# Kernel tuning notes

Measured on AMD Instinct MI355X. Metric: run time of the kernel, lower is better.

## Reference

```python
import jax, jax.numpy as jnp
import numpy as np

NSAMPLE = 16
LEAKY_RATE = 0.1


def _knn(xyz, k):
    # xyz: [B,N,3] -> idx of k nearest neighbors (incl. self): [B,N,k]
    sq = jnp.sum(xyz * xyz, axis=-1)  # [B,N]
    dist = sq[:, :, None] + sq[:, None, :] - 2.0 * jnp.einsum('bnd,bmd->bnm', xyz, xyz)
    _, idx = jax.lax.top_k(-dist, k)
    return idx


def _gather(feat, idx):
    # feat [B,N,C], idx [B,N,K] -> [B,N,K,C]
    return jax.vmap(lambda f, i: f[i])(feat, idx)


def setup_inputs() -> dict:
    key = jax.random.key(0)
    ks = jax.random.split(key, 10)
    B, N, D = 8, 4096, 61
    in_ch, out_ch, wnet = 64, 64, 16
    inp = {
        'xyz': jax.random.normal(ks[0], (B, 3, N), dtype=jnp.float32),
        'points': jax.random.normal(ks[1], (B, D, N), dtype=jnp.float32),
        # WeightNet: 1x1 convs 3->8->8->16 (hidden_unit=[8,8]), no BN
        'w0': jax.random.normal(ks[2], (8, 3), dtype=jnp.float32) * 0.3,
        'b0': jnp.zeros((8,), dtype=jnp.float32),
        'w1': jax.random.normal(ks[3], (8, 8), dtype=jnp.float32) * 0.3,
        'b1': jnp.zeros((8,), dtype=jnp.float32),
        'w2': jax.random.normal(ks[4], (wnet, 8), dtype=jnp.float32) * 0.3,
        'b2': jnp.zeros((wnet,), dtype=jnp.float32),
        # final Linear: weightnet*in_channel -> out_channel (torch [out,in] layout)
        'lin_w': jax.random.normal(ks[5], (out_ch, wnet * in_ch), dtype=jnp.float32) * 0.03,
        'lin_b': jnp.zeros((out_ch,), dtype=jnp.float32),
    }
    return inp


def reference(xyz, points, w0, b0, w1, b1, w2, b2, lin_w, lin_b):
    B, _, N = xyz.shape
    xyz_t = jnp.transpose(xyz, (0, 2, 1))     # [B,N,3]
    pts_t = jnp.transpose(points, (0, 2, 1))  # [B,N,D]
    idx = _knn(xyz_t, NSAMPLE)                # [B,N,K]
    g_xyz = _gather(xyz_t, idx) - xyz_t[:, :, None, :]   # [B,N,K,3] relative coords
    g_pts = _gather(pts_t, idx)                           # [B,N,K,D]
    new_points = jnp.concatenate([g_xyz, g_pts], axis=-1)  # [B,N,K,C], C=D+3
    # WeightNet: per-neighbor 1x1-conv MLP with ReLU on relative coords
    h = jax.nn.relu(jnp.einsum('bnkc,oc->bnko', g_xyz, w0) + b0)
    h = jax.nn.relu(jnp.einsum('bnkc,oc->bnko', h, w1) + b1)
    w = jax.nn.relu(jnp.einsum('bnkc,oc->bnko', h, w2) + b2)  # [B,N,K,W]
    # aggregate: [B,N,C,K] @ [B,N,K,W] -> [B,N,C,W] -> flatten C*W (W fastest)
    agg = jnp.einsum('bnkc,bnkw->bncw', new_points, w).reshape(B, N, -1)
    out = agg @ lin_w.T + lin_b          # [B,N,out_ch]
    out = jnp.transpose(out, (0, 2, 1))  # [B,out_ch,N]
    return jnp.where(out > 0, out, LEAKY_RATE * out)  # LeakyReLU(0.1)
```

## Files before the change

### kernel.cpp

```cpp
#include <hip/hip_runtime.h>
#include <hip/hip_bf16.h>

#define NBATCH 8
#define NP     4096
#define ND     61
#define NK     16
#define BN     (NBATCH*NP)

#define OFF_XYZT  0
#define OFF_IDX   (OFF_XYZT + BN*16)
#define OFF_PTST  (OFF_IDX + BN*64)
#define OFF_BFRAG (OFF_PTST + BN*256)

typedef __attribute__((ext_vector_type(8))) short bf16x8;
typedef __attribute__((ext_vector_type(4))) float f32x4;

static __device__ __forceinline__ unsigned short f2bf(float x) {
    unsigned int u = __float_as_uint(x);
    return (unsigned short)((u + 0x7fffu + ((u >> 16) & 1u)) >> 16);
}

__global__ __launch_bounds__(256) void k_prep_xyz(const float* __restrict__ xyz,
                                                  float4* __restrict__ xyzt) {
#pragma clang fp contract(off)
    int t = blockIdx.x * 256 + threadIdx.x;
    int b = t >> 12, n = t & (NP - 1);
    const float* base = xyz + (size_t)b * 3 * NP + n;
    float x = base[0], y = base[NP], z = base[2 * NP];
    float sq = ((x * x) + (y * y)) + (z * z);
    xyzt[t] = make_float4(x, y, z, sq);
}

__global__ __launch_bounds__(256) void k_prep_ptst(const float* __restrict__ pts,
                                                   float* __restrict__ ptst) {
    __shared__ float tile[64][65];
    int blk = blockIdx.x;
    int b = blk >> 6; int n0 = (blk & 63) << 6;
    int tid = threadIdx.x; int rg = tid >> 6; int cl = tid & 63;
#pragma unroll
    for (int d0 = 0; d0 < 64; d0 += 4) {
        int d = d0 + rg;
        if (d < ND) tile[d][cl] = pts[((size_t)b * ND + d) * NP + n0 + cl];
    }
    __syncthreads();
#pragma unroll
    for (int r = 0; r < 16; ++r) {
        int n1 = r * 4 + rg;
        float v = (cl < ND) ? tile[cl][n1] : 0.0f;
        ptst[((size_t)b * NP + n0 + n1) * 64 + cl] = v;
    }
}

__global__ __launch_bounds__(256) void k_prep_bfrag(const float* __restrict__ lw,
                                                    uint4* __restrict__ bfrag) {
    int e = blockIdx.x * 256 + threadIdx.x;
    int lane = e & 63, nt = (e >> 6) & 3, ks = e >> 8;
    int k0 = ks * 32 + (lane >> 4) * 8;
    int n = nt * 16 + (lane & 15);
    const float* src = lw + (size_t)n * 1024 + k0;
    unsigned int pk[4];
#pragma unroll
    for (int i = 0; i < 4; ++i)
        pk[i] = ((unsigned int)f2bf(src[2 * i + 1]) << 16) | f2bf(src[2 * i]);
    bfrag[e] = make_uint4(pk[0], pk[1], pk[2], pk[3]);
}

#define INSERT16(dv, jv)                                            \
    do {                                                            \
        bd[15] = (dv); bi[15] = (jv);                               \
        _Pragma("unroll")                                           \
        for (int s_ = 15; s_ > 0; --s_) {                           \
            bool sw_ = bd[s_] < bd[s_ - 1];                         \
            float td_ = bd[s_]; int ti_ = bi[s_];                   \
            bd[s_]     = sw_ ? bd[s_ - 1] : td_;                    \
            bi[s_]     = sw_ ? bi[s_ - 1] : ti_;                    \
            bd[s_ - 1] = sw_ ? td_ : bd[s_ - 1];                    \
            bi[s_ - 1] = sw_ ? ti_ : bi[s_ - 1];                    \
        }                                                           \
    } while (0)

#define DRAIN16(basev)                                                        \
    do {                                                                      \
        for (int r_ = 0; r_ < 16; ++r_) {                                     \
            if (!__any(r_ < cnt)) break;                                      \
            if (r_ < cnt) {                                                   \
                int loc_ = ring[r_ * 64 + lane];                              \
                float4 cd_ = tile[loc_];                                      \
                float dot_ = __fadd_rn(__fadd_rn(__fmul_rn(cd_.x, me.x),      \
                                                 __fmul_rn(cd_.y, me.y)),     \
                                       __fmul_rn(cd_.z, me.z));               \
                float dist_ = __fsub_rn(__fadd_rn(me.w, cd_.w),               \
                                        __fmul_rn(2.0f, dot_));               \
                if (dist_ < bd[15]) {                                         \
                    int gj_ = (basev) + loc_;                                 \
                    INSERT16(dist_, gj_);                                     \
                }                                                             \
            }                                                                 \
        }                                                                     \
        cnt = 0;                                                              \
        T = fminf(T, (bd[15] - me.w) + 1.0e-3f);                              \
    } while (0)

#define TSYNC()                                                               \
    do {                                                                      \
        Tsh[w * 64 + lane] = bd[15];                                          \
        float tm_ = Tsh[lane];                                                \
        _Pragma("unroll")                                                     \
        for (int v_ = 1; v_ < 8; ++v_) tm_ = fminf(tm_, Tsh[v_ * 64 + lane]); \
        T = fminf(T, (tm_ - me.w) + 1.0e-3f);                                 \
    } while (0)

__global__ __launch_bounds__(512) void k_knn(const float4* __restrict__ xyzt,
                                             int* __restrict__ out) {
    __shared__ char smem[65536 + 2048];
    int tid = threadIdx.x;
    int w = tid >> 6, lane = tid & 63;
    int blk = blockIdx.x;
    int b = blk >> 6;
    int qbase = (blk & 63) << 6;
    const float4* xb = xyzt + (size_t)b * NP;

    float4* tile = (float4*)(smem + w * 4096);
    int*    ring = (int*)(smem + 32768 + w * 4096);
    float*  Tsh  = (float*)(smem + 65536);

    float4 me = xb[qbase + lane];
    float bd[16]; int bi[16];
#pragma unroll
    for (int i = 0; i < 16; ++i) { bd[i] = 3.0e38f; bi[i] = 0; }
    int cnt = 0;
    float T = 3.0e38f;
    Tsh[w * 64 + lane] = 3.0e38f;
    __syncthreads();

    int cbase = w * 512;
    for (int half = 0; half < 2; ++half) {
        int base = cbase + half * 256;
#pragma unroll
        for (int r = 0; r < 4; ++r)
            tile[lane + r * 64] = xb[base + lane + r * 64];
        for (int seg = 0; seg < 4; ++seg) {
            for (int g = 0; g < 8; ++g) {
                int j0 = seg * 64 + g * 8;
#pragma unroll
                for (int u = 0; u < 8; ++u) {
                    int jj = j0 + u;
                    float4 cd = tile[jj];
                    float dotf = fmaf(cd.z, me.z, fmaf(cd.y, me.y, cd.x * me.x));
                    float df = fmaf(-2.0f, dotf, cd.w);
                    if (df < T) { ring[cnt * 64 + lane] = jj; ++cnt; }
                }
                if (__any(cnt >= 8)) { DRAIN16(base); }
                if (half == 0 && seg == 0 && (g == 1 || g == 3)) { TSYNC(); }
            }
            TSYNC();
        }
        DRAIN16(base);
    }

    __syncthreads();
    float2* part = (float2*)smem;
#pragma unroll
    for (int e = 0; e < 16; ++e)
        part[(w * 16 + e) * 64 + lane] = make_float2(bd[e], __int_as_float(bi[e]));
    __syncthreads();

    if (w == 0) {
        float bd[16]; int bi[16];
#pragma unroll
        for (int e = 0; e < 16; ++e) {
            float2 v = part[e * 64 + lane];
            bd[e] = v.x; bi[e] = __float_as_int(v.y);
        }
        for (int s = 1; s < 8; ++s) {
#pragma unroll
            for (int e = 0; e < 16; ++e) {
                float2 v = part[(s * 16 + e) * 64 + lane];
                if (v.x >= bd[15]) break;
                float d_ = v.x; int j_ = __float_as_int(v.y);
                INSERT16(d_, j_);
            }
        }
        int4* op = (int4*)(out + ((size_t)b * NP + qbase + lane) * 16);
        op[0] = make_int4(bi[0], bi[1], bi[2], bi[3]);
        op[1] = make_int4(bi[4], bi[5], bi[6], bi[7]);
        op[2] = make_int4(bi[8], bi[9], bi[10], bi[11]);
        op[3] = make_int4(bi[12], bi[13], bi[14], bi[15]);
    }
}

__global__ __launch_bounds__(256) void k_wagg(
    const float4* __restrict__ xyzt, const int* __restrict__ knn,
    const float* __restrict__ ptst, const uint4* __restrict__ bfrag,
    const float* __restrict__ w0, const float* __restrict__ b0,
    const float* __restrict__ w1, const float* __restrict__ b1,
    const float* __restrict__ w2, const float* __restrict__ b2,
    const float* __restrict__ linb, float* __restrict__ out) {
    __shared__ float wkl[256 * 16];
    __shared__ float4 rel4[256];
    __shared__ uint4 aggL4[16 * 128];
    char* aggL = (char*)aggL4;

    int tid = threadIdx.x;
    int wid = tid >> 6, lane = tid & 63;
    int q0 = blockIdx.x * 16;
    int b = q0 >> 12;
    int n0 = q0 & (NP - 1);
    size_t bN = (size_t)b * NP;

    {
        int pw = lane >> 4, k = lane & 15;
        int p = wid * 4 + pw;
        int r = p * 16 + k;
        int q = q0 + p;
        int j = knn[(size_t)q * 16 + k];
        float4 pj = xyzt[bN + j];
        float4 pq = xyzt[q];
        float rx = pj.x - pq.x, ry = pj.y - pq.y, rz = pj.z - pq.z;
        float h0[8], h1[8], wv[16];
#pragma unroll
        for (int o = 0; o < 8; ++o) {
            float a = w0[o * 3 + 0] * rx + w0[o * 3 + 1] * ry + w0[o * 3 + 2] * rz + b0[o];
            h0[o] = a > 0.0f ? a : 0.0f;
        }
#pragma unroll
        for (int o = 0; o < 8; ++o) {
            float a = b1[o];
#pragma unroll
            for (int c2 = 0; c2 < 8; ++c2) a += w1[o * 8 + c2] * h0[c2];
            h1[o] = a > 0.0f ? a : 0.0f;
        }
#pragma unroll
        for (int o = 0; o < 16; ++o) {
            float a = b2[o];
#pragma unroll
            for (int c2 = 0; c2 < 8; ++c2) a += w2[o * 8 + c2] * h1[c2];
            wv[o] = a > 0.0f ? a : 0.0f;
        }
        int f = (r >> 1) & 3;
#pragma unroll
        for (int s = 0; s < 4; ++s)
            *(float4*)&wkl[r * 16 + ((s ^ f) << 2)] =
                make_float4(wv[s * 4], wv[s * 4 + 1], wv[s * 4 + 2], wv[s * 4 + 3]);
        rel4[r] = make_float4(rx, ry, rz, __int_as_float(j));
    }
    __syncthreads();

    for (int u = 0; u < 4; ++u) {
        int p = wid * 4 + u;
        float acc[16];
#pragma unroll
        for (int w = 0; w < 16; ++w) acc[w] = 0.0f;
#pragma unroll
        for (int k = 0; k < 16; ++k) {
            int r = p * 16 + k;
            float4 rj = rel4[r];
            int j = __float_as_int(rj.w);
            float v;
            if (lane >= 3) v = ptst[(bN + j) * 64 + (lane - 3)];
            else v = (lane == 0) ? rj.x : ((lane == 1) ? rj.y : rj.z);
            int f = (r >> 1) & 3;
#pragma unroll
            for (int s = 0; s < 4; ++s) {
                float4 wv4 = *(const float4*)&wkl[r * 16 + ((s ^ f) << 2)];
                acc[s * 4 + 0] = fmaf(v, wv4.x, acc[s * 4 + 0]);
                acc[s * 4 + 1] = fmaf(v, wv4.y, acc[s * 4 + 1]);
                acc[s * 4 + 2] = fmaf(v, wv4.z, acc[s * 4 + 2]);
                acc[s * 4 + 3] = fmaf(v, wv4.w, acc[s * 4 + 3]);
            }
        }
        unsigned int pk[8];
#pragma unroll
        for (int i = 0; i < 8; ++i)
            pk[i] = ((unsigned int)f2bf(acc[2 * i + 1]) << 16) | f2bf(acc[2 * i]);
        int cx = lane ^ (p & 7);
        *(uint4*)&aggL[p * 2048 + cx * 16]        = make_uint4(pk[0], pk[1], pk[2], pk[3]);
        *(uint4*)&aggL[p * 2048 + 1024 + cx * 16] = make_uint4(pk[4], pk[5], pk[6], pk[7]);
    }
    __syncthreads();

    f32x4 cacc = {0.0f, 0.0f, 0.0f, 0.0f};
    {
        int p_ = lane & 15, oct = lane >> 4;
        int h = oct & 1, chalf = oct >> 1;
        int pbase = p_ * 2048 + h * 1024;
        int px = p_ & 7;
#pragma unroll 4
        for (int ks = 0; ks < 32; ++ks) {
            int c = ks * 2 + chalf;
            bf16x8 av = *(const bf16x8*)&aggL[pbase + ((c ^ px) << 4)];
            bf16x8 bv = *(const bf16x8*)&bfrag[(ks * 4 + wid) * 64 + lane];
            cacc = __builtin_amdgcn_mfma_f32_16x16x32_bf16(av, bv, cacc, 0, 0, 0);
        }
    }
    __syncthreads();
    float* cout = wkl;
    {
        int o = wid * 16 + (lane & 15);
        int rbase = (lane >> 4) * 4;
#pragma unroll
        for (int reg = 0; reg < 4; ++reg)
            cout[o * 17 + rbase + reg] = cacc[reg];
    }
    __syncthreads();
    {
        int oo = tid >> 2, pq = tid & 3;
        float bias = linb[oo];
        float res[4];
#pragma unroll
        for (int e = 0; e < 4; ++e) {
            float s = cout[oo * 17 + pq * 4 + e] + bias;
            res[e] = s > 0.0f ? s : 0.1f * s;
        }
        *(float4*)&out[((size_t)(b * 64 + oo)) * NP + n0 + pq * 4] =
            make_float4(res[0], res[1], res[2], res[3]);
    }
}

extern "C" void kernel_launch(void* const* d_in, const int* in_sizes, int n_in,
                              void* d_out, int out_size, void* d_ws, size_t ws_size,
                              hipStream_t stream) {
    const float* xyz  = (const float*)d_in[0];
    const float* pts  = (const float*)d_in[1];
    const float* w0   = (const float*)d_in[2];
    const float* b0   = (const float*)d_in[3];
    const float* w1   = (const float*)d_in[4];
    const float* b1   = (const float*)d_in[5];
    const float* w2   = (const float*)d_in[6];
    const float* b2   = (const float*)d_in[7];
    const float* lw   = (const float*)d_in[8];
    const float* linb = (const float*)d_in[9];
    float* out = (float*)d_out;

    char* ws = (char*)d_ws;
    float4* xyzt  = (float4*)(ws + OFF_XYZT);
    int*    idx   = (int*)(ws + OFF_IDX);
    float*  ptst  = (float*)(ws + OFF_PTST);
    uint4*  bfrag = (uint4*)(ws + OFF_BFRAG);

    k_prep_xyz<<<BN / 256, 256, 0, stream>>>(xyz, xyzt);
    k_prep_ptst<<<NBATCH * (NP / 64), 256, 0, stream>>>(pts, ptst);
    k_prep_bfrag<<<32, 256, 0, stream>>>(lw, bfrag);
    k_knn<<<512, 512, 0, stream>>>(xyzt, idx);
    k_wagg<<<BN / 16, 256, 0, stream>>>(xyzt, idx, ptst, bfrag,
                                        w0, b0, w1, b1, w2, b2, linb, out);
    (void)in_sizes; (void)n_in; (void)out_size; (void)ws_size;
}
```

Before: 270.3 us.

## Drop LDS candidate tiles in kNN, read wave-uniform candidates from global

The kNN kernel no longer stages candidate points in shared memory. Each wave reads its wave-uniform candidates straight from global memory, with the wave index forced scalar through readfirstlane, so the loads can become broadcast scalar loads. The ring buffer shrinks to 16-bit indices, and the final merge runs in two phases through a smaller partial buffer. Together these cut LDS use to about 34KB and add a launch-bounds hint to raise occupancy. The trade-off is more global and cache traffic, and the drain step now re-reads candidates from global.

```diff
diff --git a/kernel.cpp b/kernel.cpp
--- a/kernel.cpp
+++ b/kernel.cpp
@@ -79,20 +79,20 @@
         }                                                           \
     } while (0)
 
-#define DRAIN16(basev)                                                        \
+#define DRAIN16()                                                             \
     do {                                                                      \
         for (int r_ = 0; r_ < 16; ++r_) {                                     \
             if (!__any(r_ < cnt)) break;                                      \
             if (r_ < cnt) {                                                   \
                 int loc_ = ring[r_ * 64 + lane];                              \
-                float4 cd_ = tile[loc_];                                      \
+                float4 cd_ = xb[cbase + loc_];                                \
                 float dot_ = __fadd_rn(__fadd_rn(__fmul_rn(cd_.x, me.x),      \
                                                  __fmul_rn(cd_.y, me.y)),     \
                                        __fmul_rn(cd_.z, me.z));               \
                 float dist_ = __fsub_rn(__fadd_rn(me.w, cd_.w),               \
                                         __fmul_rn(2.0f, dot_));               \
                 if (dist_ < bd[15]) {                                         \
-                    int gj_ = (basev) + loc_;                                 \
+                    int gj_ = cbase + loc_;                                   \
                     INSERT16(dist_, gj_);                                     \
                 }                                                             \
             }                                                                 \
@@ -110,19 +110,20 @@
         T = fminf(T, (tm_ - me.w) + 1.0e-3f);                                 \
     } while (0)
 
-__global__ __launch_bounds__(512) void k_knn(const float4* __restrict__ xyzt,
-                                             int* __restrict__ out) {
-    __shared__ char smem[65536 + 2048];
+__global__ __launch_bounds__(512, 8) void k_knn(const float4* __restrict__ xyzt,
+                                                int* __restrict__ out) {
+    __shared__ char smem[34816];
     int tid = threadIdx.x;
-    int w = tid >> 6, lane = tid & 63;
+    int w = __builtin_amdgcn_readfirstlane(tid >> 6);
+    int lane = tid & 63;
     int blk = blockIdx.x;
     int b = blk >> 6;
     int qbase = (blk & 63) << 6;
     const float4* xb = xyzt + (size_t)b * NP;
 
-    float4* tile = (float4*)(smem + w * 4096);
-    int*    ring = (int*)(smem + 32768 + w * 4096);
-    float*  Tsh  = (float*)(smem + 65536);
+    unsigned short* ring = (unsigned short*)(smem + w * 2048);
+    float* Tsh = (float*)(smem + 32768);
+    float2* part = (float2*)smem;
 
     float4 me = xb[qbase + lane];
     float bd[16]; int bi[16];
@@ -134,45 +135,48 @@
     __syncthreads();
 
     int cbase = w * 512;
-    for (int half = 0; half < 2; ++half) {
-        int base = cbase + half * 256;
-#pragma unroll
-        for (int r = 0; r < 4; ++r)
-            tile[lane + r * 64] = xb[base + lane + r * 64];
-        for (int seg = 0; seg < 4; ++seg) {
-            for (int g = 0; g < 8; ++g) {
-                int j0 = seg * 64 + g * 8;
-#pragma unroll
-                for (int u = 0; u < 8; ++u) {
-                    int jj = j0 + u;
-                    float4 cd = tile[jj];
-                    float dotf = fmaf(cd.z, me.z, fmaf(cd.y, me.y, cd.x * me.x));
-                    float df = fmaf(-2.0f, dotf, cd.w);
-                    if (df < T) { ring[cnt * 64 + lane] = jj; ++cnt; }
-                }
-                if (__any(cnt >= 8)) { DRAIN16(base); }
-                if (half == 0 && seg == 0 && (g == 1 || g == 3)) { TSYNC(); }
+
+    for (int g = 0; g < 64; ++g) {
+#pragma unroll
+        for (int u = 0; u < 8; ++u) {
+            int jj = g * 8 + u;
+            float4 cd = xb[cbase + jj];
+            float dotf = fmaf(cd.z, me.z, fmaf(cd.y, me.y, cd.x * me.x));
+            float df = fmaf(-2.0f, dotf, cd.w);
+            if (df < T) { ring[cnt * 64 + lane] = (unsigned short)jj; ++cnt; }
+        }
+        if (__any(cnt >= 8)) { DRAIN16(); }
+        if (g == 1 || g == 3 || (g & 7) == 7) { TSYNC(); }
+    }
+    DRAIN16();
+
+    __syncthreads();
+    if (w < 4) {
+#pragma unroll
+        for (int e = 0; e < 16; ++e)
+            part[(w * 16 + e) * 64 + lane] = make_float2(bd[e], __int_as_float(bi[e]));
+    }
+    __syncthreads();
+    if (w == 0) {
+        for (int s = 1; s < 4; ++s) {
+#pragma unroll
+            for (int e = 0; e < 16; ++e) {
+                float2 v = part[(s * 16 + e) * 64 + lane];
+                if (v.x >= bd[15]) break;
+                float d_ = v.x; int j_ = __float_as_int(v.y);
+                INSERT16(d_, j_);
             }
-            TSYNC();
-        }
-        DRAIN16(base);
-    }
-
-    __syncthreads();
-    float2* part = (float2*)smem;
-#pragma unroll
-    for (int e = 0; e < 16; ++e)
-        part[(w * 16 + e) * 64 + lane] = make_float2(bd[e], __int_as_float(bi[e]));
-    __syncthreads();
-
+        }
+    }
+    __syncthreads();
+    if (w >= 4) {
+#pragma unroll
+        for (int e = 0; e < 16; ++e)
+            part[((w - 4) * 16 + e) * 64 + lane] = make_float2(bd[e], __int_as_float(bi[e]));
+    }
+    __syncthreads();
     if (w == 0) {
-        float bd[16]; int bi[16];
-#pragma unroll
-        for (int e = 0; e < 16; ++e) {
-            float2 v = part[e * 64 + lane];
-            bd[e] = v.x; bi[e] = __float_as_int(v.y);
-        }
-        for (int s = 1; s < 8; ++s) {
+        for (int s = 0; s < 4; ++s) {
 #pragma unroll
             for (int e = 0; e < 16; ++e) {
                 float2 v = part[(s * 16 + e) * 64 + lane];
```

Measured after the change: 289.0 us. 6.9% more time.
